# Kernel tuning notes

Hardware: AMD Instinct MI355X
Metric: run time of the kernel (lower is better)

Reference implementation:

```python
import jax, jax.numpy as jnp
import numpy as np

N, E, IN_DIM, HID, L, H = 50000, 1600000, 32, 128, 3, 4
O = HID // H  # 32 per-head out_feats
PI = 3.141592653589793


def _glorot(key, shape):
    fan_in, fan_out = shape[-2], shape[-1]
    s = jnp.sqrt(6.0 / (fan_in + fan_out))
    return jax.random.uniform(key, shape, jnp.float32, -s, s)


def setup_inputs() -> dict:
    key = jax.random.key(0)
    ks = jax.random.split(key, 32)
    inp = {
        'node_feats': jax.random.normal(ks[0], (N, IN_DIM), jnp.float32),
        'src': jax.random.randint(ks[1], (E,), 0, N, jnp.int32),
        'dst': jax.random.randint(ks[2], (E,), 0, N, jnp.int32),
        # input projection
        'W_in': _glorot(ks[3], (IN_DIM, HID)), 'b_in': jnp.zeros((HID,), jnp.float32),
        # per-layer GATv2 params, stacked over L layers
        'W_src': _glorot(ks[4], (L, HID, HID)), 'b_src': jnp.zeros((L, HID), jnp.float32),
        'W_dst': _glorot(ks[5], (L, HID, HID)), 'b_dst': jnp.zeros((L, HID), jnp.float32),
        'attn': _glorot(ks[6], (L, H, O)),
        'ln_g': jnp.ones((L, HID), jnp.float32), 'ln_b': jnp.zeros((L, HID), jnp.float32),
        # node MLP + heads
        'W1': _glorot(ks[7], (HID, HID)), 'b1': jnp.zeros((HID,), jnp.float32),
        'W2': _glorot(ks[8], (HID, HID)), 'b2': jnp.zeros((HID,), jnp.float32),
        'Wa': _glorot(ks[9], (HID, 2)), 'ba': jnp.zeros((2,), jnp.float32),
        'Wg': _glorot(ks[10], (HID, 1)), 'bg': jnp.zeros((1,), jnp.float32),
        'Wal': _glorot(ks[11], (HID, 1)), 'bal': jnp.zeros((1,), jnp.float32),
        'Wn': _glorot(ks[12], (HID, 1)), 'bn': jnp.zeros((1,), jnp.float32),
        'Wt': _glorot(ks[13], (HID, 1)), 'bt': jnp.zeros((1,), jnp.float32),
    }
    return inp


def _segment_softmax(scores, seg, n):
    m = jax.ops.segment_max(scores, seg, num_segments=n)
    m = jnp.where(jnp.isfinite(m), m, 0.0)
    e = jnp.exp(scores - m[seg])
    s = jax.ops.segment_sum(e, seg, num_segments=n)
    return e / (s[seg] + 1e-9)


def _gatv2_layer(h, src, dst, Ws, bs, Wd, bd, a, g, b):
    n = h.shape[0]
    hs = (h @ Ws + bs).reshape(n, H, O)   # feat_src [N,H,O]
    hd = (h @ Wd + bd).reshape(n, H, O)   # feat_dst [N,H,O]
    e = jax.nn.leaky_relu(hs[src] + hd[dst], 0.2)     # [E,H,O]
    sc = jnp.einsum('eho,ho->eh', e, a)               # attention scores
    al = _segment_softmax(sc, dst, n)                 # softmax over in-edges
    rst = jax.ops.segment_sum(al[:, :, None] * hs[src], dst, num_segments=n)
    rst = rst + h.reshape(n, H, O)        # GATv2 residual (identity res_fc)
    h_new = rst.reshape(n, HID)
    x = h + h_new                         # encoder residual (dropout=eval)
    mu = jnp.mean(x, -1, keepdims=True)
    var = jnp.var(x, -1, keepdims=True)
    x = (x - mu) / jnp.sqrt(var + 1e-5) * g + b       # LayerNorm
    return jax.nn.relu(x)


def _forward(node_feats, src, dst, W_in, b_in, W_src, b_src, W_dst, b_dst, attn,
             ln_g, ln_b, W1, b1, W2, b2, Wa, ba, Wg, bg, Wal, bal, Wn, bn, Wt, bt):
    n = node_feats.shape[0]
    loops = jnp.arange(n, dtype=src.dtype)            # dgl.add_self_loop
    s = jnp.concatenate([src, loops])
    d = jnp.concatenate([dst, loops])
    h = node_feats @ W_in + b_in
    for l in range(L):
        h = _gatv2_layer(h, s, d, W_src[l], b_src[l], W_dst[l], b_dst[l],
                         attn[l], ln_g[l], ln_b[l])
    graph_emb = jnp.mean(h, axis=0, keepdims=True)    # dgl.mean_nodes, batch=1
    node_emb = h
    z = jax.nn.relu(jax.nn.relu(node_emb @ W1 + b1) @ W2 + b2)
    action_logits = z @ Wa + ba
    gamma = 5.0 * jax.nn.sigmoid((z @ Wg + bg)[:, 0])
    alpha = 2.0 * jax.nn.sigmoid((z @ Wal + bal)[:, 0])
    noise = 1.0 * jax.nn.sigmoid((z @ Wn + bn)[:, 0])
    theta = jnp.tanh((z @ Wt + bt)[:, 0]) * PI
    spawn_params = jnp.stack([gamma, alpha, noise, theta], axis=-1)
    return graph_emb, node_emb, action_logits, spawn_params


def reference(node_feats, src, dst, W_in, b_in, W_src, b_src, W_dst, b_dst, attn,
              ln_g, ln_b, W1, b1, W2, b2, Wa, ba, Wg, bg, Wal, bal, Wn, bn, Wt, bt):
    return _forward(node_feats, src, dst, W_in, b_in, W_src, b_src, W_dst, b_dst,
                    attn, ln_g, ln_b, W1, b1, W2, b2, Wa, ba, Wg, bg, Wal, bal,
                    Wn, bn, Wt, bt)
```

## Files before the change

### kernel.cpp

```cpp
#include <hip/hip_runtime.h>
#include <hip/hip_bf16.h>

#define HID 128
#define NHEAD 4

typedef __attribute__((ext_vector_type(8))) short bf16x8;
typedef __attribute__((ext_vector_type(4))) float f32x4;
typedef __attribute__((ext_vector_type(2))) float f32x2;

#define TILE 4096
__global__ __launch_bounds__(256) void partition_edges(
    const int* __restrict__ src, const int* __restrict__ dst,
    int* __restrict__ deg, int* __restrict__ tails,
    uint2* __restrict__ buckets, int BCAP, int E, int qg, int ntiles) {
    __shared__ int hist[8];
    __shared__ int base_sh[8];
    __shared__ int claim[8];
    for (int t = blockIdx.x; t < ntiles; t += gridDim.x) {
        int e0 = t * TILE;
        if (threadIdx.x < 8) { hist[threadIdx.x] = 0; claim[threadIdx.x] = 0; }
        __syncthreads();
        int dreg[16];
        int greg[16];
#pragma unroll
        for (int j = 0; j < 16; ++j) {
            int off = j * 256 + (int)threadIdx.x;
            int idx = e0 + off;
            int d = (idx < E) ? dst[idx] : -1;
            dreg[j] = d;
            int g = (d >= 0) ? (d / qg) : -1;
            greg[j] = g;
            if (g >= 0) atomicAdd(&hist[g], 1);
        }
        __syncthreads();
        if (threadIdx.x < 8)
            base_sh[threadIdx.x] = atomicAdd(&tails[threadIdx.x], hist[threadIdx.x]);
        __syncthreads();
#pragma unroll
        for (int j = 0; j < 16; ++j) {
            int g = greg[j];
            if (g >= 0) {
                int idx = e0 + j * 256 + (int)threadIdx.x;
                int s = src[idx];
                int r = atomicAdd(&claim[g], 1);
                int pos = base_sh[g] + r;
                if (pos < BCAP)
                    buckets[(size_t)g * BCAP + pos] = make_uint2((unsigned)s, (unsigned)dreg[j]);
                atomicAdd(&deg[dreg[j]], 1);
            }
        }
        __syncthreads();
    }
}

__global__ void block_sums(const int* __restrict__ deg, int* __restrict__ bsum, int n) {
    __shared__ int sbuf[512];
    int tid = threadIdx.x;
    int i = blockIdx.x * 512 + tid;
    sbuf[tid] = (i < n) ? deg[i] : 0;
    __syncthreads();
    for (int d = 256; d > 0; d >>= 1) {
        if (tid < d) sbuf[tid] += sbuf[tid + d];
        __syncthreads();
    }
    if (tid == 0) bsum[blockIdx.x] = sbuf[0];
}

__global__ void scan_partials(const int* __restrict__ bsum, int* __restrict__ bpre, int P) {
    __shared__ int buf[128];
    int tid = threadIdx.x;
    int v = (tid < P) ? bsum[tid] : 0;
    buf[tid] = v;
    __syncthreads();
    for (int d = 1; d < 128; d <<= 1) {
        int t = (tid >= d) ? buf[tid - d] : 0;
        __syncthreads();
        buf[tid] += t;
        __syncthreads();
    }
    if (tid < P) bpre[tid] = buf[tid] - v;
}

__global__ void scan_blocks(const int* __restrict__ deg, const int* __restrict__ bpre,
                            int* __restrict__ offs, int* __restrict__ woff, int n) {
    __shared__ int sbuf[512];
    int tid = threadIdx.x;
    int i = blockIdx.x * 512 + tid;
    int v = (i < n) ? deg[i] : 0;
    sbuf[tid] = v;
    __syncthreads();
    for (int d = 1; d < 512; d <<= 1) {
        int t = (tid >= d) ? sbuf[tid - d] : 0;
        __syncthreads();
        sbuf[tid] += t;
        __syncthreads();
    }
    if (i < n) {
        int incl = bpre[blockIdx.x] + sbuf[tid];
        offs[i + 1] = incl;
        woff[i] = incl - v;
    }
    if (i == 0) offs[0] = 0;
}

__global__ __launch_bounds__(256) void fill_from_buckets(
    const uint2* __restrict__ buckets, const int* __restrict__ tails,
    int* __restrict__ woff, int* __restrict__ csr_src, int BCAP) {
    int g = blockIdx.x & 7;
    int blk = blockIdx.x >> 3;
    int nblk = gridDim.x >> 3;
    int cnt = tails[g];
    if (cnt > BCAP) cnt = BCAP;
    const uint2* b = buckets + (size_t)g * BCAP;
    for (int i = blk * 256 + threadIdx.x; i < cnt; i += nblk * 256) {
        uint2 e = b[i];
        int pos = atomicAdd(&woff[e.y], 1);
        csr_src[pos] = (int)e.x;
    }
}

__device__ __forceinline__ unsigned pack2_bf16_rne(float lo, float hi) {
    unsigned a = __float_as_uint(lo);
    a = (a + 0x7fffu + ((a >> 16) & 1u)) >> 16;
    unsigned b = __float_as_uint(hi);
    b = (b + 0x7fffu + ((b >> 16) & 1u)) & 0xffff0000u;
    return a | b;
}

__device__ __forceinline__ unsigned short bf16_rne(float x) {
    unsigned u = __float_as_uint(x);
    u = (u + 0x7fffu + ((u >> 16) & 1u)) >> 16;
    return (unsigned short)u;
}

__device__ __forceinline__ f32x2 unpack_bf(unsigned u) {
    f32x2 r;
    r.x = __uint_as_float(u << 16);
    r.y = __uint_as_float(u & 0xffff0000u);
    return r;
}

__device__ __forceinline__ f32x2 leaky2(f32x2 q) {
    return __builtin_elementwise_max(q, q * 0.2f);
}

__device__ __forceinline__ float row_sum4(float x) {
    x += __int_as_float(__builtin_amdgcn_update_dpp(0, __float_as_int(x), 0xB1, 0xF, 0xF, true));
    x += __int_as_float(__builtin_amdgcn_update_dpp(0, __float_as_int(x), 0x4E, 0xF, 0xF, true));
    return x;
}

__global__ void prep_weights(const float* __restrict__ W_src, const float* __restrict__ W_dst,
                             const float* __restrict__ W1, const float* __restrict__ W2,
                             unsigned short* __restrict__ Wt) {
    int mat = blockIdx.x;
    const float* Wf = (mat < 3) ? (W_src + (size_t)mat * 16384)
                    : (mat < 6) ? (W_dst + (size_t)(mat - 3) * 16384)
                    : (mat == 6) ? W1 : W2;
    unsigned short* out = Wt + (size_t)mat * 16384;
    for (int idx = threadIdx.x; idx < 16384; idx += blockDim.x) {
        int k = idx >> 7, nn = idx & 127;
        out[nn * 128 + k] = bf16_rne(Wf[idx]);
    }
}

#define GR 64
template <int K, bool RELU, bool F32OUT, bool BF16OUT>
__global__ __launch_bounds__(256) void gemm_k(const float* __restrict__ A,
                                              const float* __restrict__ W,
                                              const float* __restrict__ bias,
                                              float* __restrict__ Cf,
                                              unsigned short* __restrict__ C16, int n) {
    __shared__ __align__(16) float a_sh[GR * K];
    const int tid = threadIdx.x;
    const int tx = tid & 31;
    const int ty = tid >> 5;
    const int r0 = blockIdx.x * GR;

    for (int i = tid * 4; i < GR * K; i += 1024) {
        int r = i / K, k = i % K;
        int gr = r0 + r;
        float4 v = make_float4(0.f, 0.f, 0.f, 0.f);
        if (gr < n) v = *(const float4*)&A[(size_t)gr * K + k];
        *(float4*)&a_sh[i] = v;
    }
    __syncthreads();

    float4 acc[8];
#pragma unroll
    for (int r = 0; r < 8; ++r) acc[r] = make_float4(0.f, 0.f, 0.f, 0.f);

    const float* ab = &a_sh[ty * 8 * K];
    const float* wb = &W[tx * 4];

    for (int k = 0; k < K; k += 4) {
        float4 w0 = *(const float4*)&wb[(size_t)(k + 0) * 128];
        float4 w1 = *(const float4*)&wb[(size_t)(k + 1) * 128];
        float4 w2 = *(const float4*)&wb[(size_t)(k + 2) * 128];
        float4 w3 = *(const float4*)&wb[(size_t)(k + 3) * 128];
#pragma unroll
        for (int r = 0; r < 8; ++r) {
            float4 a4 = *(const float4*)&ab[r * K + k];
            acc[r].x = fmaf(a4.x, w0.x, acc[r].x);
            acc[r].y = fmaf(a4.x, w0.y, acc[r].y);
            acc[r].z = fmaf(a4.x, w0.z, acc[r].z);
            acc[r].w = fmaf(a4.x, w0.w, acc[r].w);
            acc[r].x = fmaf(a4.y, w1.x, acc[r].x);
            acc[r].y = fmaf(a4.y, w1.y, acc[r].y);
            acc[r].z = fmaf(a4.y, w1.z, acc[r].z);
            acc[r].w = fmaf(a4.y, w1.w, acc[r].w);
            acc[r].x = fmaf(a4.z, w2.x, acc[r].x);
            acc[r].y = fmaf(a4.z, w2.y, acc[r].y);
            acc[r].z = fmaf(a4.z, w2.z, acc[r].z);
            acc[r].w = fmaf(a4.z, w2.w, acc[r].w);
            acc[r].x = fmaf(a4.w, w3.x, acc[r].x);
            acc[r].y = fmaf(a4.w, w3.y, acc[r].y);
            acc[r].z = fmaf(a4.w, w3.z, acc[r].z);
            acc[r].w = fmaf(a4.w, w3.w, acc[r].w);
        }
    }

    float4 b4 = *(const float4*)&bias[tx * 4];
#pragma unroll
    for (int r = 0; r < 8; ++r) {
        int gr = r0 + ty * 8 + r;
        if (gr < n) {
            float4 o;
            o.x = acc[r].x + b4.x;
            o.y = acc[r].y + b4.y;
            o.z = acc[r].z + b4.z;
            o.w = acc[r].w + b4.w;
            if (RELU) {
                o.x = fmaxf(o.x, 0.f); o.y = fmaxf(o.y, 0.f);
                o.z = fmaxf(o.z, 0.f); o.w = fmaxf(o.w, 0.f);
            }
            if (F32OUT) *(float4*)&Cf[(size_t)gr * 128 + tx * 4] = o;
            if (BF16OUT) {
                uint2 st;
                st.x = pack2_bf16_rne(o.x, o.y);
                st.y = pack2_bf16_rne(o.z, o.w);
                *(uint2*)&C16[(size_t)gr * 128 + tx * 4] = st;
            }
        }
    }
}

template <bool RELU, bool F32OUT, bool BF16OUT>
__global__ __launch_bounds__(256) void gemm_mfma(
    const unsigned short* __restrict__ A16,
    const unsigned short* __restrict__ Bt16,
    const float* __restrict__ bias,
    float* __restrict__ Cf, unsigned short* __restrict__ C16, int n) {
    const int wave = threadIdx.x >> 6;
    const int lane = threadIdx.x & 63;
    const int r = lane & 15, g = lane >> 4;
    const int m0 = blockIdx.x * 64 + wave * 16;
    int ra = m0 + r; if (ra > n - 1) ra = n - 1;
    const bf16x8* Arow = (const bf16x8*)(A16 + (size_t)ra * 128);
    bf16x8 a0 = Arow[g];
    bf16x8 a1 = Arow[4 + g];
    bf16x8 a2 = Arow[8 + g];
    bf16x8 a3 = Arow[12 + g];
#pragma unroll
    for (int ct = 0; ct < 8; ++ct) {
        const bf16x8* Brow = (const bf16x8*)(Bt16 + (size_t)(ct * 16 + r) * 128);
        f32x4 acc = {0.f, 0.f, 0.f, 0.f};
        acc = __builtin_amdgcn_mfma_f32_16x16x32_bf16(a0, Brow[g], acc, 0, 0, 0);
        acc = __builtin_amdgcn_mfma_f32_16x16x32_bf16(a1, Brow[4 + g], acc, 0, 0, 0);
        acc = __builtin_amdgcn_mfma_f32_16x16x32_bf16(a2, Brow[8 + g], acc, 0, 0, 0);
        acc = __builtin_amdgcn_mfma_f32_16x16x32_bf16(a3, Brow[12 + g], acc, 0, 0, 0);
        const int col = ct * 16 + r;
        const float bcol = bias[col];
#pragma unroll
        for (int j = 0; j < 4; ++j) {
            int row = m0 + g * 4 + j;
            if (row < n) {
                float v = acc[j] + bcol;
                if (RELU) v = fmaxf(v, 0.f);
                if (F32OUT) Cf[(size_t)row * 128 + col] = v;
                if (BF16OUT) C16[(size_t)row * 128 + col] = bf16_rne(v);
            }
        }
    }
}

__global__ __launch_bounds__(256) void gemm_mfma_dual(
    const unsigned short* __restrict__ A16,
    const unsigned short* __restrict__ B1t, const unsigned short* __restrict__ B2t,
    const float* __restrict__ bias1, const float* __restrict__ bias2,
    unsigned short* __restrict__ C1, unsigned short* __restrict__ C2, int n) {
    const int wave = threadIdx.x >> 6;
    const int lane = threadIdx.x & 63;
    const int r = lane & 15, g = lane >> 4;
    const int m0 = blockIdx.x * 64 + wave * 16;
    int ra = m0 + r; if (ra > n - 1) ra = n - 1;
    const bf16x8* Arow = (const bf16x8*)(A16 + (size_t)ra * 128);
    bf16x8 a0 = Arow[g];
    bf16x8 a1 = Arow[4 + g];
    bf16x8 a2 = Arow[8 + g];
    bf16x8 a3 = Arow[12 + g];
#pragma unroll
    for (int ct = 0; ct < 8; ++ct) {
        const int col = ct * 16 + r;
        {
            const bf16x8* Brow = (const bf16x8*)(B1t + (size_t)col * 128);
            f32x4 acc = {0.f, 0.f, 0.f, 0.f};
            acc = __builtin_amdgcn_mfma_f32_16x16x32_bf16(a0, Brow[g], acc, 0, 0, 0);
            acc = __builtin_amdgcn_mfma_f32_16x16x32_bf16(a1, Brow[4 + g], acc, 0, 0, 0);
            acc = __builtin_amdgcn_mfma_f32_16x16x32_bf16(a2, Brow[8 + g], acc, 0, 0, 0);
            acc = __builtin_amdgcn_mfma_f32_16x16x32_bf16(a3, Brow[12 + g], acc, 0, 0, 0);
            const float bcol = bias1[col];
#pragma unroll
            for (int j = 0; j < 4; ++j) {
                int row = m0 + g * 4 + j;
                if (row < n) C1[(size_t)row * 128 + col] = bf16_rne(acc[j] + bcol);
            }
        }
        {
            const bf16x8* Brow = (const bf16x8*)(B2t + (size_t)col * 128);
            f32x4 acc = {0.f, 0.f, 0.f, 0.f};
            acc = __builtin_amdgcn_mfma_f32_16x16x32_bf16(a0, Brow[g], acc, 0, 0, 0);
            acc = __builtin_amdgcn_mfma_f32_16x16x32_bf16(a1, Brow[4 + g], acc, 0, 0, 0);
            acc = __builtin_amdgcn_mfma_f32_16x16x32_bf16(a2, Brow[8 + g], acc, 0, 0, 0);
            acc = __builtin_amdgcn_mfma_f32_16x16x32_bf16(a3, Brow[12 + g], acc, 0, 0, 0);
            const float bcol = bias2[col];
#pragma unroll
            for (int j = 0; j < 4; ++j) {
                int row = m0 + g * 4 + j;
                if (row < n) C2[(size_t)row * 128 + col] = bf16_rne(acc[j] + bcol);
            }
        }
    }
}

__global__ __launch_bounds__(256) void gat_aggregate(
    const float* __restrict__ h,
    const unsigned short* __restrict__ hs16,
    const unsigned short* __restrict__ hd16,
    const int* __restrict__ offs,
    const int* __restrict__ csr_src,
    const float* __restrict__ attn,
    const float* __restrict__ ln_g, const float* __restrict__ ln_b,
    float* __restrict__ h_out, unsigned* __restrict__ h16_out, int n) {
    int v = (blockIdx.x * blockDim.x + threadIdx.x) >> 6;
    int lane = threadIdx.x & 63;
    if (v >= n) return;
    const int lh = lane & 15;
    const int quarter = lane >> 4;
    const int f0 = lh * 8;
    const unsigned fb = (unsigned)lh << 4;

    const float L2E = 1.4426950408889634f;
    f32x2 av0, av1, av2, av3;
    {
        float4 aa = *(const float4*)&attn[f0];
        float4 ab = *(const float4*)&attn[f0 + 4];
        av0 = (f32x2){aa.x, aa.y} * L2E; av1 = (f32x2){aa.z, aa.w} * L2E;
        av2 = (f32x2){ab.x, ab.y} * L2E; av3 = (f32x2){ab.z, ab.w} * L2E;
    }
    const char* hsb = (const char*)hs16;
    f32x2 hd0, hd1, hd2, hd3;
    {
        uint4 wd = *(const uint4*)((const char*)hd16 + ((size_t)(unsigned)v << 8) + fb);
        hd0 = unpack_bf(wd.x); hd1 = unpack_bf(wd.y);
        hd2 = unpack_bf(wd.z); hd3 = unpack_bf(wd.w);
    }
    uint4 wv = *(const uint4*)(hsb + ((size_t)(unsigned)v << 8) + fb);
    f32x2 sv0 = unpack_bf(wv.x), sv1 = unpack_bf(wv.y);
    f32x2 sv2 = unpack_bf(wv.z), sv3 = unpack_bf(wv.w);
    float m;
    {
        f32x2 q0 = leaky2(sv0 + hd0), q1 = leaky2(sv1 + hd1);
        f32x2 q2 = leaky2(sv2 + hd2), q3 = leaky2(sv3 + hd3);
        f32x2 dt = q0 * av0; dt += q1 * av1; dt += q2 * av2; dt += q3 * av3;
        m = row_sum4(dt.x + dt.y);
    }
    const bool q0lane = (quarter == 0);
    float s = q0lane ? 1.f : 0.f;
    f32x2 acc0 = q0lane ? sv0 : (f32x2){0.f, 0.f};
    f32x2 acc1 = q0lane ? sv1 : (f32x2){0.f, 0.f};
    f32x2 acc2 = q0lane ? sv2 : (f32x2){0.f, 0.f};
    f32x2 acc3 = q0lane ? sv3 : (f32x2){0.f, 0.f};

    int beg = offs[v], end = offs[v + 1];
    int end4 = beg + ((end - beg) & ~3);

    auto process = [&](uint4 w) {
        f32x2 g0 = unpack_bf(w.x), g1 = unpack_bf(w.y);
        f32x2 g2 = unpack_bf(w.z), g3 = unpack_bf(w.w);
        f32x2 p0 = leaky2(g0 + hd0), p1 = leaky2(g1 + hd1);
        f32x2 p2 = leaky2(g2 + hd2), p3 = leaky2(g3 + hd3);
        f32x2 dt = p0 * av0; dt += p1 * av1; dt += p2 * av2; dt += p3 * av3;
        float sc = row_sum4(dt.x + dt.y);
        float d0 = sc - m;
        if (__builtin_expect(__any(d0 > 8.f), 0)) {
            float dmx = fmaxf(d0, __shfl_xor(d0, 16));
            dmx = fmaxf(dmx, __shfl_xor(dmx, 32));
            float mn = m + fmaxf(dmx, 0.f);
            float rr = exp2f(m - mn);
            s *= rr; acc0 *= rr; acc1 *= rr; acc2 *= rr; acc3 *= rr;
            m = mn; d0 = sc - m;
        }
        float e = exp2f(d0);
        s += e;
        acc0 += g0 * e; acc1 += g1 * e; acc2 += g2 * e; acc3 += g3 * e;
    };

    if (end4 > beg) {
        uint4 w = *(const uint4*)(hsb + ((size_t)(unsigned)csr_src[beg + quarter] << 8) + fb);
        int un = (beg + 4 < end4) ? csr_src[beg + 4 + quarter] : 0;
        for (int i = beg + 4; i < end4; i += 4) {
            uint4 wn = *(const uint4*)(hsb + ((size_t)(unsigned)un << 8) + fb);
            if (i + 4 < end4) un = csr_src[i + 4 + quarter];
            process(w);
            w = wn;
        }
        process(w);
    }
    if (end4 < end) {
        int idx = end4 + quarter;
        bool act = idx < end;
        int u = csr_src[act ? idx : end4];
        uint4 w = *(const uint4*)(hsb + ((size_t)(unsigned)u << 8) + fb);
        f32x2 g0 = unpack_bf(w.x), g1 = unpack_bf(w.y);
        f32x2 g2 = unpack_bf(w.z), g3 = unpack_bf(w.w);
        f32x2 p0 = leaky2(g0 + hd0), p1 = leaky2(g1 + hd1);
        f32x2 p2 = leaky2(g2 + hd2), p3 = leaky2(g3 + hd3);
        f32x2 dt = p0 * av0; dt += p1 * av1; dt += p2 * av2; dt += p3 * av3;
        float sc = row_sum4(dt.x + dt.y);
        float d0 = sc - m;
        float d0m = act ? d0 : -1e30f;
        if (__builtin_expect(__any(d0m > 8.f), 0)) {
            float dmx = fmaxf(d0m, __shfl_xor(d0m, 16));
            dmx = fmaxf(dmx, __shfl_xor(dmx, 32));
            float mn = m + fmaxf(dmx, 0.f);
            float rr = exp2f(m - mn);
            s *= rr; acc0 *= rr; acc1 *= rr; acc2 *= rr; acc3 *= rr;
            m = mn; d0 = sc - m;
        }
        float e = act ? exp2f(d0) : 0.f;
        s += e;
        acc0 += g0 * e; acc1 += g1 * e; acc2 += g2 * e; acc3 += g3 * e;
    }
#pragma unroll
    for (int d = 16; d <= 32; d <<= 1) {
        s += __shfl_xor(s, d);
        acc0.x += __shfl_xor(acc0.x, d); acc0.y += __shfl_xor(acc0.y, d);
        acc1.x += __shfl_xor(acc1.x, d); acc1.y += __shfl_xor(acc1.y, d);
        acc2.x += __shfl_xor(acc2.x, d); acc2.y += __shfl_xor(acc2.y, d);
        acc3.x += __shfl_xor(acc3.x, d); acc3.y += __shfl_xor(acc3.y, d);
    }
    float inv = 1.0f / (s + 1e-9f);

    f32x2 hv0, hv1, hv2, hv3;
    {
        float4 ha = *(const float4*)&h[(size_t)v * 128 + f0];
        float4 hb = *(const float4*)&h[(size_t)v * 128 + f0 + 4];
        hv0 = (f32x2){ha.x, ha.y}; hv1 = (f32x2){ha.z, ha.w};
        hv2 = (f32x2){hb.x, hb.y}; hv3 = (f32x2){hb.z, hb.w};
    }
    f32x2 x0 = acc0 * inv + hv0 * 2.f;
    f32x2 x1 = acc1 * inv + hv1 * 2.f;
    f32x2 x2 = acc2 * inv + hv2 * 2.f;
    f32x2 x3 = acc3 * inv + hv3 * 2.f;

    f32x2 sum2 = (x0 + x1) + (x2 + x3);
    f32x2 sq2 = x0 * x0 + x1 * x1 + x2 * x2 + x3 * x3;
    float sum = sum2.x + sum2.y, sq = sq2.x + sq2.y;
#pragma unroll
    for (int d = 1; d < 64; d <<= 1) { sum += __shfl_xor(sum, d); sq += __shfl_xor(sq, d); }
    float mu = sum * (1.f / 512.f);
    float var = sq * (1.f / 512.f) - mu * mu;
    float rstd = rsqrtf(var + 1e-5f);
    f32x2 g0v, g1v, g2v, g3v, b0v, b1v, b2v, b3v;
    {
        float4 ga = *(const float4*)&ln_g[f0];
        float4 gb = *(const float4*)&ln_g[f0 + 4];
        float4 ba = *(const float4*)&ln_b[f0];
        float4 bb = *(const float4*)&ln_b[f0 + 4];
        g0v = (f32x2){ga.x, ga.y}; g1v = (f32x2){ga.z, ga.w};
        g2v = (f32x2){gb.x, gb.y}; g3v = (f32x2){gb.z, gb.w};
        b0v = (f32x2){ba.x, ba.y}; b1v = (f32x2){ba.z, ba.w};
        b2v = (f32x2){bb.x, bb.y}; b3v = (f32x2){bb.z, bb.w};
    }
    f32x2 zero = {0.f, 0.f};
    f32x2 y0 = __builtin_elementwise_max((x0 - mu) * rstd * g0v + b0v, zero);
    f32x2 y1 = __builtin_elementwise_max((x1 - mu) * rstd * g1v + b1v, zero);
    f32x2 y2 = __builtin_elementwise_max((x2 - mu) * rstd * g2v + b2v, zero);
    f32x2 y3 = __builtin_elementwise_max((x3 - mu) * rstd * g3v + b3v, zero);
    if (quarter == 0) {
        float* orow = &h_out[(size_t)v * 128 + f0];
        *(float4*)orow = make_float4(y0.x, y0.y, y1.x, y1.y);
        *(float4*)(orow + 4) = make_float4(y2.x, y2.y, y3.x, y3.y);
        uint4 st;
        st.x = pack2_bf16_rne(y0.x, y0.y);
        st.y = pack2_bf16_rne(y1.x, y1.y);
        st.z = pack2_bf16_rne(y2.x, y2.y);
        st.w = pack2_bf16_rne(y3.x, y3.y);
        *(uint4*)((char*)h16_out + ((size_t)v << 8) + fb) = st;
    }
}

__global__ __launch_bounds__(256) void mean_partial(const float4* __restrict__ src,
                                                    float* __restrict__ gacc, size_t n4) {
    int tid = threadIdx.x;
    size_t i = blockIdx.x * (size_t)256 + tid;
    size_t stride = (size_t)gridDim.x * 256;
    float ax = 0.f, ay = 0.f, az = 0.f, aw = 0.f;
    for (; i < n4; i += stride) {
        float4 v = src[i];
        ax += v.x; ay += v.y; az += v.z; aw += v.w;
    }
    __shared__ float4 sb[256];
    sb[tid] = make_float4(ax, ay, az, aw);
    __syncthreads();
    for (int off = 128; off >= 32; off >>= 1) {
        if (tid < off) {
            float4 o = sb[tid + off];
            sb[tid].x += o.x; sb[tid].y += o.y; sb[tid].z += o.z; sb[tid].w += o.w;
        }
        __syncthreads();
    }
    if (tid < 32) {
        float4 a = sb[tid];
        atomicAdd(&gacc[tid * 4 + 0], a.x);
        atomicAdd(&gacc[tid * 4 + 1], a.y);
        atomicAdd(&gacc[tid * 4 + 2], a.z);
        atomicAdd(&gacc[tid * 4 + 3], a.w);
    }
}

__global__ void graph_mean_final(const float* __restrict__ gacc, float* __restrict__ out, int n) {
    int c = threadIdx.x;
    out[c] = gacc[c] / (float)n;
}

__global__ __launch_bounds__(256) void heads_kernel(
    const float* __restrict__ z,
    const float* __restrict__ Wa, const float* __restrict__ ba,
    const float* __restrict__ Wg, const float* __restrict__ bg,
    const float* __restrict__ Wal, const float* __restrict__ bal,
    const float* __restrict__ Wn, const float* __restrict__ bn,
    const float* __restrict__ Wt, const float* __restrict__ bt,
    float* __restrict__ logits, float* __restrict__ spawn, int n) {
    int v = (blockIdx.x * blockDim.x + threadIdx.x) >> 6;
    int lane = threadIdx.x & 63;
    if (v >= n) return;
    int f0 = lane * 2;
    float2 zv = *(const float2*)&z[(size_t)v * 128 + f0];
    float p0 = zv.x * Wa[f0 * 2]     + zv.y * Wa[(f0 + 1) * 2];
    float p1 = zv.x * Wa[f0 * 2 + 1] + zv.y * Wa[(f0 + 1) * 2 + 1];
    float p2 = zv.x * Wg[f0]  + zv.y * Wg[f0 + 1];
    float p3 = zv.x * Wal[f0] + zv.y * Wal[f0 + 1];
    float p4 = zv.x * Wn[f0]  + zv.y * Wn[f0 + 1];
    float p5 = zv.x * Wt[f0]  + zv.y * Wt[f0 + 1];
#pragma unroll
    for (int d = 1; d < 64; d <<= 1) {
        p0 += __shfl_xor(p0, d); p1 += __shfl_xor(p1, d); p2 += __shfl_xor(p2, d);
        p3 += __shfl_xor(p3, d); p4 += __shfl_xor(p4, d); p5 += __shfl_xor(p5, d);
    }
    if (lane == 0) {
        logits[(size_t)v * 2 + 0] = p0 + ba[0];
        logits[(size_t)v * 2 + 1] = p1 + ba[1];
        float gamma = 5.f / (1.f + __expf(-(p2 + bg[0])));
        float alpha = 2.f / (1.f + __expf(-(p3 + bal[0])));
        float noise = 1.f / (1.f + __expf(-(p4 + bn[0])));
        float theta = tanhf(p5 + bt[0]) * 3.14159265358979323846f;
        spawn[(size_t)v * 4 + 0] = gamma;
        spawn[(size_t)v * 4 + 1] = alpha;
        spawn[(size_t)v * 4 + 2] = noise;
        spawn[(size_t)v * 4 + 3] = theta;
    }
}

extern "C" void kernel_launch(void* const* d_in, const int* in_sizes, int n_in,
                              void* d_out, int out_size, void* d_ws, size_t ws_size,
                              hipStream_t stream) {
    const float* node_feats = (const float*)d_in[0];
    const int*   src  = (const int*)d_in[1];
    const int*   dst  = (const int*)d_in[2];
    const float* W_in = (const float*)d_in[3];
    const float* b_in = (const float*)d_in[4];
    const float* W_src = (const float*)d_in[5];
    const float* b_src = (const float*)d_in[6];
    const float* W_dst = (const float*)d_in[7];
    const float* b_dst = (const float*)d_in[8];
    const float* attn  = (const float*)d_in[9];
    const float* ln_g  = (const float*)d_in[10];
    const float* ln_b  = (const float*)d_in[11];
    const float* W1 = (const float*)d_in[12]; const float* b1 = (const float*)d_in[13];
    const float* W2 = (const float*)d_in[14]; const float* b2 = (const float*)d_in[15];
    const float* Wa = (const float*)d_in[16]; const float* ba = (const float*)d_in[17];
    const float* Wg = (const float*)d_in[18]; const float* bg = (const float*)d_in[19];
    const float* Wal = (const float*)d_in[20]; const float* bal = (const float*)d_in[21];
    const float* Wn = (const float*)d_in[22]; const float* bn = (const float*)d_in[23];
    const float* Wt = (const float*)d_in[24]; const float* bt = (const float*)d_in[25];

    const int n = in_sizes[0] / 32;
    const int E = in_sizes[1];
    const int P = (n + 511) / 512;
    const int qg = (n + 7) / 8;
    const int BCAP = 240 * 1024;
    const int ntiles = (E + TILE - 1) / TILE;

    char* ws = (char*)d_ws;
    size_t off = 0;
    auto alloc = [&](size_t bytes) -> void* {
        void* p = ws + off;
        off = (off + bytes + 255) & ~(size_t)255;
        return p;
    };
    float* Bh0 = (float*)alloc((size_t)n * 128 * 4);
    float* Bh1 = (float*)alloc((size_t)n * 128 * 4);
    float* Bz  = (float*)alloc((size_t)n * 128 * 4);
    unsigned short* h16  = (unsigned short*)alloc((size_t)n * 128 * 2);
    unsigned short* hs16 = (unsigned short*)alloc((size_t)n * 128 * 2);
    unsigned short* hd16 = (unsigned short*)alloc((size_t)n * 128 * 2);
    unsigned short* Wt16 = (unsigned short*)alloc((size_t)8 * 16384 * 2);
    int* deg  = (int*)alloc((size_t)n * 4);
    int* offs = (int*)alloc((size_t)(n + 1) * 4);
    int* woff = (int*)alloc((size_t)n * 4);
    int* csr  = (int*)alloc((size_t)E * 4);
    uint2* buckets = (uint2*)alloc((size_t)8 * BCAP * 8);
    int* tails = (int*)alloc(8 * 4);
    int* bsum = (int*)alloc((size_t)P * 4);
    int* bpre = (int*)alloc((size_t)P * 4);
    float* gacc = (float*)alloc(128 * 4);

    float* out = (float*)d_out;
    float* out_gemb   = out;
    float* out_nemb   = out + 128;
    float* out_logits = out + 128 + (size_t)n * 128;
    float* out_spawn  = out_logits + (size_t)n * 2;

    hipMemsetAsync(deg, 0, (size_t)n * 4, stream);
    hipMemsetAsync(tails, 0, 8 * 4, stream);
    hipMemsetAsync(gacc, 0, 128 * 4, stream);

    partition_edges<<<ntiles, 256, 0, stream>>>(src, dst, deg, tails, buckets, BCAP, E, qg, ntiles);
    block_sums<<<P, 512, 0, stream>>>(deg, bsum, n);
    scan_partials<<<1, 128, 0, stream>>>(bsum, bpre, P);
    scan_blocks<<<P, 512, 0, stream>>>(deg, bpre, offs, woff, n);
    fill_from_buckets<<<2048, 256, 0, stream>>>(buckets, tails, woff, csr, BCAP);

    prep_weights<<<8, 256, 0, stream>>>(W_src, W_dst, W1, W2, Wt16);

    int gemm_grid = (n + GR - 1) / GR;
    int mfma_grid = (n + 63) / 64;

    gemm_k<32, false, true, true><<<gemm_grid, 256, 0, stream>>>(node_feats, W_in, b_in, Bh0, h16, n);

    float* cur = Bh0;
    for (int l = 0; l < 3; ++l) {
        gemm_mfma_dual<<<mfma_grid, 256, 0, stream>>>(
            h16, Wt16 + (size_t)l * 16384, Wt16 + (size_t)(3 + l) * 16384,
            b_src + l * 128, b_dst + l * 128, hs16, hd16, n);
        float* nxt = (l == 2) ? out_nemb : ((cur == Bh0) ? Bh1 : Bh0);
        gat_aggregate<<<(n + 3) / 4, 256, 0, stream>>>(cur, hs16, hd16, offs, csr,
                                                       attn + l * 128, ln_g + l * 128,
                                                       ln_b + l * 128, nxt, (unsigned*)h16, n);
        cur = nxt;
    }

    gemm_mfma<true, false, true><<<mfma_grid, 256, 0, stream>>>(
        h16, Wt16 + (size_t)6 * 16384, b1, nullptr, hs16, n);
    gemm_mfma<true, true, false><<<mfma_grid, 256, 0, stream>>>(
        hs16, Wt16 + (size_t)7 * 16384, b2, Bz, nullptr, n);

    mean_partial<<<512, 256, 0, stream>>>((const float4*)out_nemb, gacc, (size_t)n * 32);
    graph_mean_final<<<1, 128, 0, stream>>>(gacc, out_gemb, n);
    heads_kernel<<<(n + 3) / 4, 256, 0, stream>>>(Bz, Wa, ba, Wg, bg, Wal, bal,
                                                  Wn, bn, Wt, bt, out_logits, out_spawn, n);
}
```

Measured before the change: 637.0 us.

## Replace shared-atomic edge partition with ballot ranking and separate degree count

The edge partitioning kernel now ranks edges within each bucket using wave ballots and popcounts plus a per-wave prefix. This replaces the per-edge shared-memory atomics used before and shrinks the tile to 1024 edges per block. Degree counting moves out into a new kernel that reads the buckets, so its global atomics run over destinations already grouped by bucket and hit L2 more locally. The cost is an extra kernel launch and a second pass that reads the buckets back.

```diff
diff --git a/kernel.cpp b/kernel.cpp
--- a/kernel.cpp
+++ b/kernel.cpp
@@ -8,49 +8,73 @@
 typedef __attribute__((ext_vector_type(4))) float f32x4;
 typedef __attribute__((ext_vector_type(2))) float f32x2;
 
-#define TILE 4096
+#define TILE2 1024
 __global__ __launch_bounds__(256) void partition_edges(
     const int* __restrict__ src, const int* __restrict__ dst,
-    int* __restrict__ deg, int* __restrict__ tails,
-    uint2* __restrict__ buckets, int BCAP, int E, int qg, int ntiles) {
-    __shared__ int hist[8];
+    int* __restrict__ tails, uint2* __restrict__ buckets,
+    int BCAP, int E, int qg) {
+    __shared__ int warr[4][8];
     __shared__ int base_sh[8];
-    __shared__ int claim[8];
-    for (int t = blockIdx.x; t < ntiles; t += gridDim.x) {
-        int e0 = t * TILE;
-        if (threadIdx.x < 8) { hist[threadIdx.x] = 0; claim[threadIdx.x] = 0; }
-        __syncthreads();
-        int dreg[16];
-        int greg[16];
-#pragma unroll
-        for (int j = 0; j < 16; ++j) {
-            int off = j * 256 + (int)threadIdx.x;
-            int idx = e0 + off;
-            int d = (idx < E) ? dst[idx] : -1;
-            dreg[j] = d;
-            int g = (d >= 0) ? (d / qg) : -1;
-            greg[j] = g;
-            if (g >= 0) atomicAdd(&hist[g], 1);
-        }
-        __syncthreads();
-        if (threadIdx.x < 8)
-            base_sh[threadIdx.x] = atomicAdd(&tails[threadIdx.x], hist[threadIdx.x]);
-        __syncthreads();
-#pragma unroll
-        for (int j = 0; j < 16; ++j) {
-            int g = greg[j];
-            if (g >= 0) {
-                int idx = e0 + j * 256 + (int)threadIdx.x;
-                int s = src[idx];
-                int r = atomicAdd(&claim[g], 1);
-                int pos = base_sh[g] + r;
-                if (pos < BCAP)
-                    buckets[(size_t)g * BCAP + pos] = make_uint2((unsigned)s, (unsigned)dreg[j]);
-                atomicAdd(&deg[dreg[j]], 1);
-            }
-        }
-        __syncthreads();
-    }
+    const int tid = threadIdx.x;
+    const int wave = tid >> 6, lane = tid & 63;
+    const int e0 = blockIdx.x * TILE2;
+    const unsigned long long below = (1ULL << lane) - 1ULL;
+
+    int sreg[4], dreg[4], binr[4], rankr[4];
+    int wcnt[8] = {0, 0, 0, 0, 0, 0, 0, 0};
+#pragma unroll
+    for (int j = 0; j < 4; ++j) {
+        int idx = e0 + j * 256 + tid;
+        bool ok = idx < E;
+        int d = ok ? dst[idx] : 0;
+        int s = ok ? src[idx] : 0;
+        int g = ok ? (d / qg) : -1;
+        sreg[j] = s; dreg[j] = d; binr[j] = g;
+        int r = 0;
+#pragma unroll
+        for (int b = 0; b < 8; ++b) {
+            unsigned long long mb = __ballot(g == b);
+            if (g == b) r = wcnt[b] + (int)__popcll(mb & below);
+            wcnt[b] += (int)__popcll(mb);
+        }
+        rankr[j] = r;
+    }
+    if (lane == 0) {
+#pragma unroll
+        for (int b = 0; b < 8; ++b) warr[wave][b] = wcnt[b];
+    }
+    __syncthreads();
+    if (tid < 8) {
+        int b = tid, tot = 0;
+        int pre[4];
+#pragma unroll
+        for (int w = 0; w < 4; ++w) { pre[w] = tot; tot += warr[w][b]; }
+        base_sh[b] = atomicAdd(&tails[b], tot);
+#pragma unroll
+        for (int w = 0; w < 4; ++w) warr[w][b] = pre[w];
+    }
+    __syncthreads();
+#pragma unroll
+    for (int j = 0; j < 4; ++j) {
+        int g = binr[j];
+        if (g >= 0) {
+            int pos = base_sh[g] + warr[wave][g] + rankr[j];
+            if (pos < BCAP)
+                buckets[(size_t)g * BCAP + pos] = make_uint2((unsigned)sreg[j], (unsigned)dreg[j]);
+        }
+    }
+}
+
+__global__ __launch_bounds__(256) void count_from_buckets(
+    const uint2* __restrict__ buckets, const int* __restrict__ tails,
+    int* __restrict__ deg, int BCAP) {
+    int g = blockIdx.x & 7;
+    int blk = blockIdx.x >> 3;
+    int nblk = gridDim.x >> 3;
+    int cnt = tails[g]; if (cnt > BCAP) cnt = BCAP;
+    const uint2* b = buckets + (size_t)g * BCAP;
+    for (int i = blk * 256 + threadIdx.x; i < cnt; i += nblk * 256)
+        atomicAdd(&deg[b[i].y], 1);
 }
 
 __global__ void block_sums(const int* __restrict__ deg, int* __restrict__ bsum, int n) {
@@ -601,7 +625,7 @@
     const int P = (n + 511) / 512;
     const int qg = (n + 7) / 8;
     const int BCAP = 240 * 1024;
-    const int ntiles = (E + TILE - 1) / TILE;
+    const int ntiles = (E + TILE2 - 1) / TILE2;
 
     char* ws = (char*)d_ws;
     size_t off = 0;
@@ -637,7 +661,8 @@
     hipMemsetAsync(tails, 0, 8 * 4, stream);
     hipMemsetAsync(gacc, 0, 128 * 4, stream);
 
-    partition_edges<<<ntiles, 256, 0, stream>>>(src, dst, deg, tails, buckets, BCAP, E, qg, ntiles);
+    partition_edges<<<ntiles, 256, 0, stream>>>(src, dst, tails, buckets, BCAP, E, qg);
+    count_from_buckets<<<2048, 256, 0, stream>>>(buckets, tails, deg, BCAP);
     block_sums<<<P, 512, 0, stream>>>(deg, bsum, n);
     scan_partials<<<1, 128, 0, stream>>>(bsum, bpre, P);
     scan_blocks<<<P, 512, 0, stream>>>(deg, bpre, offs, woff, n);
```

Result: no change. 648.5 us (+1.8%).
